# Kernel tuning notes

Measured on AMD Instinct MI355X. Metric: run time of the kernel, lower is better.

## Reference

```python
import jax, jax.numpy as jnp
import numpy as np
import math

D_MODEL = 1024
N_HEADS = 16
D_K = D_MODEL // N_HEADS
WIDTH_MULTIPLIER = 1.0  # readout=False on all projections, so unused in math


def setup_inputs() -> dict:
    key = jax.random.key(0)
    kx, kq, kk, kv, ko = jax.random.split(key, 5)
    std = 1.0 / math.sqrt(D_MODEL)  # init_scale=1.0 / sqrt(in_features)
    x = jax.random.normal(kx, (2, 2048, D_MODEL), dtype=jnp.float32)
    # weights stored as (out_features, in_features), matching torch
    Wq = jax.random.normal(kq, (D_MODEL, D_MODEL), dtype=jnp.float32) * std
    Wk = jax.random.normal(kk, (D_MODEL, D_MODEL), dtype=jnp.float32) * std
    Wv = jax.random.normal(kv, (D_MODEL, D_MODEL), dtype=jnp.float32) * std
    Wo = jax.random.normal(ko, (D_MODEL, D_MODEL), dtype=jnp.float32) * std
    return {"x": x, "Wq": Wq, "Wk": Wk, "Wv": Wv, "Wo": Wo}


def reference(x, Wq, Wk, Wv, Wo):
    B, S, D = x.shape
    H, Dk = N_HEADS, D_K
    # muPLinear: x @ W.T (bias=False, readout=False)
    q = jnp.einsum('bsd,ed->bse', x, Wq).reshape(B, S, H, Dk).transpose(0, 2, 1, 3)
    k = jnp.einsum('bsd,ed->bse', x, Wk).reshape(B, S, H, Dk).transpose(0, 2, 1, 3)
    v = jnp.einsum('bsd,ed->bse', x, Wv).reshape(B, S, H, Dk).transpose(0, 2, 1, 3)
    # full [B,H,S,S] scores, scaled by 1/sqrt(d_k), softmax over keys
    scores = jnp.einsum('bhqd,bhkd->bhqk', q, k) / math.sqrt(Dk)
    attn = jax.nn.softmax(scores, axis=-1)
    out = jnp.einsum('bhqk,bhkd->bhqd', attn, v)
    out = out.transpose(0, 2, 1, 3).reshape(B, S, D)
    return jnp.einsum('bsd,ed->bse', out, Wo)
```

## Files before the change

### kernel.cpp

```cpp
#include <hip/hip_runtime.h>
#include <hip/hip_bf16.h>
#include <math.h>

#define D_MODEL 1024
#define N_HEADS 16
#define D_K     64
#define BATCH   2
#define SEQ     2048
#define M_TOTAL (BATCH * SEQ)

typedef __attribute__((ext_vector_type(8))) short short8;
typedef __attribute__((ext_vector_type(4))) float f32x4;

__device__ __forceinline__ ushort f2bf(float f) {
    __hip_bfloat16 h = __float2bfloat16(f);
    union { __hip_bfloat16 h; ushort u; } c; c.h = h; return c.u;
}

__device__ __forceinline__ void gload_lds16(const void* g, void* l) {
    __builtin_amdgcn_global_load_lds(
        (const __attribute__((address_space(1))) void*)g,
        (__attribute__((address_space(3))) void*)l, 16, 0, 0);
}

__global__ __launch_bounds__(256) void cast_all(const float* __restrict__ x,
                                                const float* __restrict__ Wq,
                                                const float* __restrict__ Wk,
                                                const float* __restrict__ Wv,
                                                const float* __restrict__ Wo,
                                                ushort* __restrict__ xb,
                                                ushort* __restrict__ wqkv,
                                                ushort* __restrict__ wob)
{
    const int bi = blockIdx.x;
    const float* src; ushort* dst; int blk;
    const int NW = D_MODEL * D_MODEL;
    if (bi < 4096)      { src = x;  dst = xb;            blk = bi; }
    else if (bi < 5120) { src = Wq; dst = wqkv;          blk = bi - 4096; }
    else if (bi < 6144) { src = Wk; dst = wqkv + NW;     blk = bi - 5120; }
    else if (bi < 7168) { src = Wv; dst = wqkv + 2 * NW; blk = bi - 6144; }
    else                { src = Wo; dst = wob;           blk = bi - 7168; }
    const int i = blk * 1024 + threadIdx.x * 4;
    float4 v = *(const float4*)&src[i];
    ushort4 o;
    o.x = f2bf(v.x); o.y = f2bf(v.y); o.z = f2bf(v.z); o.w = f2bf(v.w);
    *(ushort4*)&dst[i] = o;
}

template <int EPI>
__global__ __launch_bounds__(256) void gemm_bf16(const ushort* __restrict__ A,
                                                 const ushort* __restrict__ B,
                                                 void* __restrict__ C0,
                                                 void* __restrict__ C1,
                                                 void* __restrict__ C2,
                                                 int M, int N, int K)
{
    __shared__ ushort As[2][4 * 128 * 8];
    __shared__ ushort Bs[2][4 * 128 * 8];

    const int tid = threadIdx.x;
    const int lane = tid & 63;
    const int w = tid >> 6;
    const int li = lane & 15;
    const int kg = lane >> 4;
    const int m0 = blockIdx.y * 128;
    const int n0 = blockIdx.x * 128;
    const int wr = (w >> 1) * 64;
    const int wc = (w & 1) * 64;

    f32x4 acc[4][4] = {};

    const int s1 = tid, s2 = tid + 256;
    const ushort* ga1 = &A[(size_t)(m0 + (s1 & 127)) * K + (s1 >> 7) * 8];
    const ushort* ga2 = &A[(size_t)(m0 + (s2 & 127)) * K + (s2 >> 7) * 8];
    const ushort* gb1 = &B[(size_t)(n0 + (s1 & 127)) * K + (s1 >> 7) * 8];
    const ushort* gb2 = &B[(size_t)(n0 + (s2 & 127)) * K + (s2 >> 7) * 8];

    const int NT = K / 32;
    gload_lds16(ga1, &As[0][s1 * 8]);
    gload_lds16(ga2, &As[0][s2 * 8]);
    gload_lds16(gb1, &Bs[0][s1 * 8]);
    gload_lds16(gb2, &Bs[0][s2 * 8]);

    for (int t = 0; t < NT; ++t) {
        const int cur = t & 1;
        asm volatile("s_waitcnt vmcnt(0)" ::: "memory");
        __syncthreads();
        if (t + 1 < NT) {
            const int kb = (t + 1) * 32;
            const int nxt = cur ^ 1;
            gload_lds16(ga1 + kb, &As[nxt][s1 * 8]);
            gload_lds16(ga2 + kb, &As[nxt][s2 * 8]);
            gload_lds16(gb1 + kb, &Bs[nxt][s1 * 8]);
            gload_lds16(gb2 + kb, &Bs[nxt][s2 * 8]);
        }
        short8 af[4], bf_[4];
#pragma unroll
        for (int m = 0; m < 4; ++m)
            af[m] = *(const short8*)&As[cur][(kg * 128 + wr + m * 16 + li) * 8];
#pragma unroll
        for (int n = 0; n < 4; ++n)
            bf_[n] = *(const short8*)&Bs[cur][(kg * 128 + wc + n * 16 + li) * 8];
#pragma unroll
        for (int m = 0; m < 4; ++m)
#pragma unroll
            for (int n = 0; n < 4; ++n)
                acc[m][n] = __builtin_amdgcn_mfma_f32_16x16x32_bf16(
                    af[m], bf_[n], acc[m][n], 0, 0, 0);
    }

    if (EPI == 1) {
        ushort* q = (ushort*)C0; ushort* k = (ushort*)C1; ushort* v = (ushort*)C2;
        const float QSCALE = 0.125f * 1.44269504088896f;
#pragma unroll
        for (int m = 0; m < 4; ++m) {
            const int Rb = m0 + wr + m * 16 + kg * 4;
#pragma unroll
            for (int n = 0; n < 4; ++n) {
                const int Ncol = n0 + wc + n * 16 + li;
                const int proj = Ncol >> 10;
                const int rem = Ncol & 1023;
                const int h = rem >> 6, dk = rem & 63;
#pragma unroll
                for (int r = 0; r < 4; ++r) {
                    const int R = Rb + r;
                    const int b = R >> 11, s = R & 2047;
                    const int bh = b * N_HEADS + h;
                    if (proj == 0)
                        q[((size_t)bh * SEQ + s) * D_K + dk] = f2bf(acc[m][n][r] * QSCALE);
                    else if (proj == 1)
                        k[((size_t)bh * SEQ + s) * D_K + dk] = f2bf(acc[m][n][r]);
                    else
                        v[((size_t)bh * D_K + dk) * SEQ + s] = f2bf(acc[m][n][r]);
                }
            }
        }
    } else {
        float* C = (float*)C0;
#pragma unroll
        for (int m = 0; m < 4; ++m) {
            const int Rb = m0 + wr + m * 16 + kg * 4;
#pragma unroll
            for (int n = 0; n < 4; ++n) {
                const int Ncol = n0 + wc + n * 16 + li;
#pragma unroll
                for (int r = 0; r < 4; ++r)
                    C[(size_t)(Rb + r) * N + Ncol] = acc[m][n][r];
            }
        }
    }
}

__global__ __launch_bounds__(256) void attn_mfma(const ushort* __restrict__ Q,
                                                 const ushort* __restrict__ K,
                                                 const ushort* __restrict__ Vt,
                                                 ushort* __restrict__ AO)
{
    __shared__ ushort Ks[2][64 * 64];
    __shared__ ushort Vs[2][64 * 64];
    __shared__ ushort Ps[4][16 * 64];

    const int tid = threadIdx.x, lane = tid & 63, w = tid >> 6;
    const int li = lane & 15, g = lane >> 4;
    const int b = blockIdx.z, h = blockIdx.y, q0 = blockIdx.x * 64;
    const int bh = b * N_HEADS + h;
    const size_t base = (size_t)bh * SEQ * D_K;
    const size_t vbase = (size_t)bh * D_K * SEQ;

    const size_t qrow = base + (size_t)(q0 + w * 16 + li) * D_K;
    const short8 qa0 = *(const short8*)&Q[qrow + g * 8];
    const short8 qa1 = *(const short8*)&Q[qrow + 32 + g * 8];

    float m_ = -INFINITY, l_ = 0.f;
    f32x4 o[4] = {};

    const int srow_l = lane >> 3;
    const int sblk = lane & 7;
    ushort* Pw = &Ps[w][0];
    const ushort* Kt0 = &K[base];
    const ushort* Vt0 = &Vt[vbase];

#define STAGE(kt_, buf_)                                                      \
    {                                                                         \
        _Pragma("unroll")                                                     \
        for (int p = 0; p < 2; ++p) {                                         \
            const int row = w * 16 + p * 8 + srow_l;                          \
            const int db = sblk ^ (row & 7);                                  \
            gload_lds16(Kt0 + ((size_t)((kt_) * 64 + row)) * D_K + db * 8,    \
                        &Ks[buf_][(w * 16 + p * 8) * 64]);                    \
            gload_lds16(Vt0 + (size_t)row * SEQ + (kt_) * 64 + db * 8,        \
                        &Vs[buf_][(w * 16 + p * 8) * 64]);                    \
        }                                                                     \
    }

    STAGE(0, 0);

    const int NT = SEQ / 64;
    for (int kt = 0; kt < NT; ++kt) {
        const int cur = kt & 1;
        asm volatile("s_waitcnt vmcnt(0)" ::: "memory");
        __syncthreads();
        if (kt + 1 < NT) STAGE(kt + 1, cur ^ 1);

        f32x4 s4[4];
#pragma unroll
        for (int kf = 0; kf < 4; ++kf) {
            const int row = kf * 16 + li;
            short8 kb0 = *(const short8*)&Ks[cur][row * 64 + ((g ^ (row & 7)) * 8)];
            short8 kb1 = *(const short8*)&Ks[cur][row * 64 + (((4 + g) ^ (row & 7)) * 8)];
            f32x4 z = {0.f, 0.f, 0.f, 0.f};
            z = __builtin_amdgcn_mfma_f32_16x16x32_bf16(kb0, qa0, z, 0, 0, 0);
            z = __builtin_amdgcn_mfma_f32_16x16x32_bf16(kb1, qa1, z, 0, 0, 0);
            s4[kf] = z;
        }

        f32x4 mm01, mm;
#pragma unroll
        for (int e = 0; e < 4; ++e) mm01[e] = fmaxf(s4[0][e], s4[1][e]);
#pragma unroll
        for (int e = 0; e < 4; ++e) mm[e] = fmaxf(mm01[e], fmaxf(s4[2][e], s4[3][e]));
        float mx = fmaxf(fmaxf(mm[0], mm[1]), fmaxf(mm[2], mm[3]));
        mx = fmaxf(mx, __shfl_xor(mx, 16, 64));
        mx = fmaxf(mx, __shfl_xor(mx, 32, 64));

        if (__any(mx > m_ + 8.0f)) {
            const float mn = fmaxf(m_, mx);
            const float sc = exp2f(m_ - mn);
            l_ *= sc;
#pragma unroll
            for (int df = 0; df < 4; ++df)
#pragma unroll
                for (int e = 0; e < 4; ++e) o[df][e] *= sc;
            m_ = mn;
        }

        float p[4][4];
        float ts = 0.f;
#pragma unroll
        for (int kf = 0; kf < 4; ++kf)
#pragma unroll
            for (int r = 0; r < 4; ++r) {
                p[kf][r] = exp2f(s4[kf][r] - m_);
                ts += p[kf][r];
            }
        ts += __shfl_xor(ts, 16, 64);
        ts += __shfl_xor(ts, 32, 64);
        l_ += ts;

#pragma unroll
        for (int kf = 0; kf < 4; ++kf)
#pragma unroll
            for (int rr = 0; rr < 2; ++rr) {
                const uint u = ((uint)f2bf(p[kf][2 * rr + 1]) << 16) | f2bf(p[kf][2 * rr]);
                const int blk = 2 * kf + (g >> 1);
                *(uint*)&Pw[li * 64 + ((blk ^ (li & 7)) * 8) + (g & 1) * 4 + rr * 2] = u;
            }
        asm volatile("s_waitcnt lgkmcnt(0)" ::: "memory");
        __builtin_amdgcn_sched_barrier(0);

        const short8 pb0 = *(const short8*)&Pw[li * 64 + ((g ^ (li & 7)) * 8)];
        const short8 pb1 = *(const short8*)&Pw[li * 64 + (((4 + g) ^ (li & 7)) * 8)];
#pragma unroll
        for (int df = 0; df < 4; ++df) {
            const int row = df * 16 + li;
            short8 vb0 = *(const short8*)&Vs[cur][row * 64 + ((g ^ (row & 7)) * 8)];
            short8 vb1 = *(const short8*)&Vs[cur][row * 64 + (((4 + g) ^ (row & 7)) * 8)];
            o[df] = __builtin_amdgcn_mfma_f32_16x16x32_bf16(vb0, pb0, o[df], 0, 0, 0);
            o[df] = __builtin_amdgcn_mfma_f32_16x16x32_bf16(vb1, pb1, o[df], 0, 0, 0);
        }
    }
#undef STAGE

    const float inv = 1.0f / l_;
    ushort* Ao = &AO[((size_t)b * SEQ + q0 + w * 16 + li) * D_MODEL + h * 64];
#pragma unroll
    for (int df = 0; df < 4; ++df)
#pragma unroll
        for (int rr = 0; rr < 2; ++rr) {
            const uint u = ((uint)f2bf(o[df][2 * rr + 1] * inv) << 16) |
                           f2bf(o[df][2 * rr] * inv);
            *(uint*)&Ao[df * 16 + g * 4 + rr * 2] = u;
        }
}

extern "C" void kernel_launch(void* const* d_in, const int* in_sizes, int n_in,
                              void* d_out, int out_size, void* d_ws, size_t ws_size,
                              hipStream_t stream)
{
    const float* x  = (const float*)d_in[0];
    const float* Wq = (const float*)d_in[1];
    const float* Wk = (const float*)d_in[2];
    const float* Wv = (const float*)d_in[3];
    const float* Wo = (const float*)d_in[4];
    float* out = (float*)d_out;

    ushort* xb   = (ushort*)d_ws;
    ushort* Wqkv = xb + (size_t)M_TOTAL * D_MODEL;
    ushort* Wob  = Wqkv + (size_t)3 * D_MODEL * D_MODEL;
    ushort* q    = Wob + (size_t)D_MODEL * D_MODEL;
    ushort* k    = q + (size_t)M_TOTAL * D_MODEL;
    ushort* vt   = k + (size_t)M_TOTAL * D_MODEL;
    ushort* ao   = vt + (size_t)M_TOTAL * D_MODEL;

    hipLaunchKernelGGL(cast_all, dim3(8192), dim3(256), 0, stream,
                       x, Wq, Wk, Wv, Wo, xb, Wqkv, Wob);

    hipLaunchKernelGGL((gemm_bf16<1>), dim3(3 * D_MODEL / 128, M_TOTAL / 128), dim3(256),
                       0, stream, xb, Wqkv, q, k, vt, M_TOTAL, 3 * D_MODEL, D_MODEL);

    hipLaunchKernelGGL(attn_mfma, dim3(SEQ / 64, N_HEADS, BATCH), dim3(256),
                       0, stream, q, k, vt, ao);

    hipLaunchKernelGGL((gemm_bf16<0>), dim3(D_MODEL / 128, M_TOTAL / 128), dim3(256),
                       0, stream, ao, Wob, out, (void*)0, (void*)0,
                       M_TOTAL, D_MODEL, D_MODEL);
}
```

Baseline: 191.7 us.

## Switch attention to 32x32 MFMA with register-resident P via permlane swaps

Rewrites the attention inner loop to use 32x32x16 bf16 MFMA, with each wave handling 32 query rows and each block 128 queries. The softmax probabilities are now rearranged in registers with v_permlane32_swap instead of being written to and read back from LDS, which removes the per-tile LDS round trip and its wait. A runtime probe picks the swap operand order. The change doubles K/V reuse per block and halves the grid, at the cost of more accumulator registers and possibly lower occupancy.

New measurement: 187.5 us. 2.2% less time.

```diff
diff --git a/kernel.cpp b/kernel.cpp
--- a/kernel.cpp
+++ b/kernel.cpp
@@ -11,16 +11,25 @@
 
 typedef __attribute__((ext_vector_type(8))) short short8;
 typedef __attribute__((ext_vector_type(4))) float f32x4;
+typedef __attribute__((ext_vector_type(16))) float f32x16;
 
 __device__ __forceinline__ ushort f2bf(float f) {
     __hip_bfloat16 h = __float2bfloat16(f);
     union { __hip_bfloat16 h; ushort u; } c; c.h = h; return c.u;
+}
+
+__device__ __forceinline__ uint packbf(float a, float b) {
+    return ((uint)f2bf(b) << 16) | (uint)f2bf(a);
 }
 
 __device__ __forceinline__ void gload_lds16(const void* g, void* l) {
     __builtin_amdgcn_global_load_lds(
         (const __attribute__((address_space(1))) void*)g,
         (__attribute__((address_space(3))) void*)l, 16, 0, 0);
+}
+
+__device__ __forceinline__ void plswap(uint& a, uint& b) {
+    asm volatile("v_permlane32_swap_b32 %0, %1" : "+v"(a), "+v"(b));
 }
 
 __global__ __launch_bounds__(256) void cast_all(const float* __restrict__ x,
@@ -158,25 +167,29 @@
 {
     __shared__ ushort Ks[2][64 * 64];
     __shared__ ushort Vs[2][64 * 64];
-    __shared__ ushort Ps[4][16 * 64];
 
     const int tid = threadIdx.x, lane = tid & 63, w = tid >> 6;
-    const int li = lane & 15, g = lane >> 4;
-    const int b = blockIdx.z, h = blockIdx.y, q0 = blockIdx.x * 64;
+    const int r31 = lane & 31, hi = lane >> 5;
+    const int b = blockIdx.z, h = blockIdx.y, q0 = blockIdx.x * 128;
     const int bh = b * N_HEADS + h;
     const size_t base = (size_t)bh * SEQ * D_K;
     const size_t vbase = (size_t)bh * D_K * SEQ;
 
-    const size_t qrow = base + (size_t)(q0 + w * 16 + li) * D_K;
-    const short8 qa0 = *(const short8*)&Q[qrow + g * 8];
-    const short8 qa1 = *(const short8*)&Q[qrow + 32 + g * 8];
+    uint pa = (uint)lane, pbv = 1000u + (uint)lane;
+    plswap(pa, pbv);
+    const bool swap_lo = (__builtin_amdgcn_readfirstlane(pa) > 500u);
+
+    const size_t qrow = base + (size_t)(q0 + w * 32 + r31) * D_K;
+    short8 qb[4];
+#pragma unroll
+    for (int ks = 0; ks < 4; ++ks)
+        qb[ks] = *(const short8*)&Q[qrow + ks * 16 + hi * 8];
 
     float m_ = -INFINITY, l_ = 0.f;
-    f32x4 o[4] = {};
+    f32x16 o0 = {}, o1 = {};
 
     const int srow_l = lane >> 3;
     const int sblk = lane & 7;
-    ushort* Pw = &Ps[w][0];
     const ushort* Kt0 = &K[base];
     const ushort* Vt0 = &Vt[vbase];
 
@@ -202,25 +215,25 @@
         __syncthreads();
         if (kt + 1 < NT) STAGE(kt + 1, cur ^ 1);
 
-        f32x4 s4[4];
-#pragma unroll
-        for (int kf = 0; kf < 4; ++kf) {
-            const int row = kf * 16 + li;
-            short8 kb0 = *(const short8*)&Ks[cur][row * 64 + ((g ^ (row & 7)) * 8)];
-            short8 kb1 = *(const short8*)&Ks[cur][row * 64 + (((4 + g) ^ (row & 7)) * 8)];
-            f32x4 z = {0.f, 0.f, 0.f, 0.f};
-            z = __builtin_amdgcn_mfma_f32_16x16x32_bf16(kb0, qa0, z, 0, 0, 0);
-            z = __builtin_amdgcn_mfma_f32_16x16x32_bf16(kb1, qa1, z, 0, 0, 0);
-            s4[kf] = z;
-        }
-
-        f32x4 mm01, mm;
-#pragma unroll
-        for (int e = 0; e < 4; ++e) mm01[e] = fmaxf(s4[0][e], s4[1][e]);
-#pragma unroll
-        for (int e = 0; e < 4; ++e) mm[e] = fmaxf(mm01[e], fmaxf(s4[2][e], s4[3][e]));
-        float mx = fmaxf(fmaxf(mm[0], mm[1]), fmaxf(mm[2], mm[3]));
-        mx = fmaxf(mx, __shfl_xor(mx, 16, 64));
+        f32x16 s0 = {}, s1 = {};
+#pragma unroll
+        for (int ks = 0; ks < 4; ++ks) {
+            const int row = r31;
+            short8 kb = *(const short8*)&Ks[cur][row * 64 + (((2 * ks + hi) ^ (row & 7)) * 8)];
+            s0 = __builtin_amdgcn_mfma_f32_32x32x16_bf16(kb, qb[ks], s0, 0, 0, 0);
+        }
+#pragma unroll
+        for (int ks = 0; ks < 4; ++ks) {
+            const int row = 32 + r31;
+            short8 kb = *(const short8*)&Ks[cur][row * 64 + (((2 * ks + hi) ^ (row & 7)) * 8)];
+            s1 = __builtin_amdgcn_mfma_f32_32x32x16_bf16(kb, qb[ks], s1, 0, 0, 0);
+        }
+
+        float mx = fmaxf(s0[0], s0[1]);
+#pragma unroll
+        for (int e = 2; e < 16; ++e) mx = fmaxf(mx, s0[e]);
+#pragma unroll
+        for (int e = 0; e < 16; ++e) mx = fmaxf(mx, s1[e]);
         mx = fmaxf(mx, __shfl_xor(mx, 32, 64));
 
         if (__any(mx > m_ + 8.0f)) {
@@ -228,59 +241,67 @@
             const float sc = exp2f(m_ - mn);
             l_ *= sc;
 #pragma unroll
-            for (int df = 0; df < 4; ++df)
-#pragma unroll
-                for (int e = 0; e < 4; ++e) o[df][e] *= sc;
+            for (int e = 0; e < 16; ++e) { o0[e] *= sc; o1[e] *= sc; }
             m_ = mn;
         }
 
-        float p[4][4];
+        f32x16 p0, p1;
         float ts = 0.f;
 #pragma unroll
-        for (int kf = 0; kf < 4; ++kf)
-#pragma unroll
-            for (int r = 0; r < 4; ++r) {
-                p[kf][r] = exp2f(s4[kf][r] - m_);
-                ts += p[kf][r];
-            }
-        ts += __shfl_xor(ts, 16, 64);
+        for (int e = 0; e < 16; ++e) { p0[e] = exp2f(s0[e] - m_); ts += p0[e]; }
+#pragma unroll
+        for (int e = 0; e < 16; ++e) { p1[e] = exp2f(s1[e] - m_); ts += p1[e]; }
         ts += __shfl_xor(ts, 32, 64);
         l_ += ts;
 
-#pragma unroll
-        for (int kf = 0; kf < 4; ++kf)
-#pragma unroll
-            for (int rr = 0; rr < 2; ++rr) {
-                const uint u = ((uint)f2bf(p[kf][2 * rr + 1]) << 16) | f2bf(p[kf][2 * rr]);
-                const int blk = 2 * kf + (g >> 1);
-                *(uint*)&Pw[li * 64 + ((blk ^ (li & 7)) * 8) + (g & 1) * 4 + rr * 2] = u;
-            }
-        asm volatile("s_waitcnt lgkmcnt(0)" ::: "memory");
-        __builtin_amdgcn_sched_barrier(0);
-
-        const short8 pb0 = *(const short8*)&Pw[li * 64 + ((g ^ (li & 7)) * 8)];
-        const short8 pb1 = *(const short8*)&Pw[li * 64 + (((4 + g) ^ (li & 7)) * 8)];
-#pragma unroll
-        for (int df = 0; df < 4; ++df) {
-            const int row = df * 16 + li;
-            short8 vb0 = *(const short8*)&Vs[cur][row * 64 + ((g ^ (row & 7)) * 8)];
-            short8 vb1 = *(const short8*)&Vs[cur][row * 64 + (((4 + g) ^ (row & 7)) * 8)];
-            o[df] = __builtin_amdgcn_mfma_f32_16x16x32_bf16(vb0, pb0, o[df], 0, 0, 0);
-            o[df] = __builtin_amdgcn_mfma_f32_16x16x32_bf16(vb1, pb1, o[df], 0, 0, 0);
+        uint u[8][2];
+#pragma unroll
+        for (int rq = 0; rq < 4; ++rq) {
+            u[rq][0]     = packbf(p0[4 * rq + 0], p0[4 * rq + 1]);
+            u[rq][1]     = packbf(p0[4 * rq + 2], p0[4 * rq + 3]);
+            u[4 + rq][0] = packbf(p1[4 * rq + 0], p1[4 * rq + 1]);
+            u[4 + rq][1] = packbf(p1[4 * rq + 2], p1[4 * rq + 3]);
+        }
+
+        short8 pb[4];
+#pragma unroll
+        for (int ks = 0; ks < 4; ++ks) {
+            uint x0 = u[2 * ks][0], x1 = u[2 * ks][1];
+            uint y0 = u[2 * ks + 1][0], y1 = u[2 * ks + 1][1];
+            if (swap_lo) { plswap(y0, x0); plswap(y1, x1); }
+            else         { plswap(x0, y0); plswap(x1, y1); }
+            union { uint u4[4]; short8 s; } pu;
+            pu.u4[0] = x0; pu.u4[1] = x1; pu.u4[2] = y0; pu.u4[3] = y1;
+            pb[ks] = pu.s;
+        }
+
+#pragma unroll
+        for (int ks = 0; ks < 4; ++ks) {
+            const int row = r31;
+            short8 vb = *(const short8*)&Vs[cur][row * 64 + (((2 * ks + hi) ^ (row & 7)) * 8)];
+            o0 = __builtin_amdgcn_mfma_f32_32x32x16_bf16(vb, pb[ks], o0, 0, 0, 0);
+        }
+#pragma unroll
+        for (int ks = 0; ks < 4; ++ks) {
+            const int row = 32 + r31;
+            short8 vb = *(const short8*)&Vs[cur][row * 64 + (((2 * ks + hi) ^ (row & 7)) * 8)];
+            o1 = __builtin_amdgcn_mfma_f32_32x32x16_bf16(vb, pb[ks], o1, 0, 0, 0);
         }
     }
 #undef STAGE
 
     const float inv = 1.0f / l_;
-    ushort* Ao = &AO[((size_t)b * SEQ + q0 + w * 16 + li) * D_MODEL + h * 64];
-#pragma unroll
-    for (int df = 0; df < 4; ++df)
-#pragma unroll
-        for (int rr = 0; rr < 2; ++rr) {
-            const uint u = ((uint)f2bf(o[df][2 * rr + 1] * inv) << 16) |
-                           f2bf(o[df][2 * rr] * inv);
-            *(uint*)&Ao[df * 16 + g * 4 + rr * 2] = u;
-        }
+    ushort* Ao = &AO[((size_t)b * SEQ + q0 + w * 32 + r31) * D_MODEL + h * 64];
+#pragma unroll
+    for (int rq = 0; rq < 4; ++rq) {
+        uint2 v0, v1;
+        v0.x = packbf(o0[4 * rq + 0] * inv, o0[4 * rq + 1] * inv);
+        v0.y = packbf(o0[4 * rq + 2] * inv, o0[4 * rq + 3] * inv);
+        v1.x = packbf(o1[4 * rq + 0] * inv, o1[4 * rq + 1] * inv);
+        v1.y = packbf(o1[4 * rq + 2] * inv, o1[4 * rq + 3] * inv);
+        *(uint2*)&Ao[8 * rq + 4 * hi]      = v0;
+        *(uint2*)&Ao[32 + 8 * rq + 4 * hi] = v1;
+    }
 }
 
 extern "C" void kernel_launch(void* const* d_in, const int* in_sizes, int n_in,
@@ -308,7 +329,7 @@
     hipLaunchKernelGGL((gemm_bf16<1>), dim3(3 * D_MODEL / 128, M_TOTAL / 128), dim3(256),
                        0, stream, xb, Wqkv, q, k, vt, M_TOTAL, 3 * D_MODEL, D_MODEL);
 
-    hipLaunchKernelGGL(attn_mfma, dim3(SEQ / 64, N_HEADS, BATCH), dim3(256),
+    hipLaunchKernelGGL(attn_mfma, dim3(SEQ / 128, N_HEADS, BATCH), dim3(256),
                        0, stream, q, k, vt, ao);
 
     hipLaunchKernelGGL((gemm_bf16<0>), dim3(D_MODEL / 128, M_TOTAL / 128), dim3(256),
```
